# Optimization experiments

Hardware: AMD Instinct MI355X
Metric: run time of the kernel (lower is better)

## Reference

```python
import jax, jax.numpy as jnp
import numpy as np

C, B, F, O, DK = 10, 8192, 256, 64, 5


def setup_inputs() -> dict:
    key = jax.random.key(0)
    ks = jax.random.split(key, 7)
    x = jax.random.normal(ks[0], (B, F), jnp.float32)
    y = jax.random.normal(ks[1], (B, C), jnp.float32)
    # kaiming-uniform-like init scales
    w_key = jax.random.normal(ks[2], (C, 1, 1, DK), jnp.float32) * 0.5
    w_query = jax.random.normal(ks[3], (C, 1, DK), jnp.float32) * 0.5
    w_value = jax.random.normal(ks[4], (C, 1, 1), jnp.float32) * 0.5
    weight = jax.random.normal(ks[5], (C, 1, F, O), jnp.float32) * (1.0 / np.sqrt(F))
    bias = jax.random.normal(ks[6], (C, 1, O), jnp.float32) * 0.1
    return {"x": x, "y": y, "w_key": w_key, "w_query": w_query,
            "w_value": w_value, "weight": weight, "bias": bias}


def reference(x, y, w_key, w_query, w_value, weight, bias):
    # x: [B,F] (first=True -> conceptually [1,B,F]); y: [B,C]
    yt = y.T                                             # [C,B]
    querys = yt[..., None] * w_query                     # [C,B,1]*[C,1,DK] -> [C,B,DK]
    # keys[c,b,f,k] = x[b,f] * w_key[c,k]; attn_scores[c,b,f] = sum_k keys*querys
    #              = x[b,f] * (w_key[c] . querys[c,b])  (rank-1 structure, fused)
    kq = jnp.einsum('ck,cbk->cb', w_key.reshape(w_key.shape[0], -1), querys)  # [C,B]
    # mean over batch dim, then softmax over features
    scores_avg = jnp.einsum('bf,cb->cf', x, kq) / x.shape[0]  # [C,F]
    sm = jax.nn.softmax(scores_avg, axis=-1)                  # [C,F]
    attn = sm / jnp.max(sm, axis=-1, keepdims=True)           # [C,F] max-normalized
    values = x[None, :, :] * w_value                          # [1,B,F]*[C,1,1] -> [C,B,F]
    weighted = values * attn[:, None, :]                      # [C,B,F]
    # (weighted[...,None,:] @ weight).squeeze() + bias -> [C,B,O]
    out = jnp.einsum('cbf,cfo->cbo', weighted, weight[:, 0]) + bias  # bias [C,1,O]
    return out
```

## Files before the change

### kernel.cpp

```cpp
#include <hip/hip_runtime.h>
#include <hip/hip_bf16.h>

#define C_ 10
#define B_ 8192
#define F_ 256
#define O_ 64
#define DK_ 5
#define NBLK1 256
#define NG2   16

typedef __attribute__((ext_vector_type(8))) short short8;
typedef __attribute__((ext_vector_type(4))) float floatx4;

static __device__ __forceinline__ unsigned short f2bf(float f) {
    union { float f; unsigned u; } v; v.f = f;
    unsigned r = v.u + 0x7fffu + ((v.u >> 16) & 1u);
    return (unsigned short)(r >> 16);
}

__global__ __launch_bounds__(256) void k1_reduce(const float* __restrict__ x,
                                                 const float* __restrict__ y,
                                                 float* __restrict__ G_part) {
    __shared__ float xl[32 * F_];
    __shared__ float yl[32 * C_];
    const int b0 = blockIdx.x * 32;
    const int t  = threadIdx.x;

    for (int i = t; i < 32 * C_; i += 256) yl[i] = y[b0 * C_ + i];

    const int r  = t >> 6;
    const int f4 = (t & 63) * 4;
#pragma unroll
    for (int j = 0; j < 8; ++j) {
        int row = r + 4 * j;
        float4 v = *(const float4*)(x + (size_t)(b0 + row) * F_ + f4);
        *(float4*)(xl + row * F_ + f4) = v;
    }
    __syncthreads();

    float acc[C_];
#pragma unroll
    for (int c = 0; c < C_; ++c) acc[c] = 0.f;

#pragma unroll 8
    for (int b = 0; b < 32; ++b) {
        float xv = xl[b * F_ + t];
#pragma unroll
        for (int c = 0; c < C_; ++c) acc[c] = fmaf(yl[b * C_ + c], xv, acc[c]);
    }

    float* gp = G_part + (size_t)blockIdx.x * C_ * F_ + t;
#pragma unroll
    for (int c = 0; c < C_; ++c) gp[c * F_] = acc[c];
}

__global__ __launch_bounds__(256) void k1b_reduce(const float* __restrict__ G_part,
                                                  const float* __restrict__ weight,
                                                  float* __restrict__ G2,
                                                  unsigned short* __restrict__ WTB) {
    const int c = (int)blockIdx.x >> 4;
    const int g = (int)blockIdx.x & 15;
    const int t = threadIdx.x;

    const float* gp = G_part + (size_t)(g * 16) * C_ * F_ + c * F_ + t;
    float a0 = 0.f, a1 = 0.f, a2 = 0.f, a3 = 0.f;
#pragma unroll
    for (int i = 0; i < 16; i += 4) {
        a0 += gp[(size_t)(i + 0) * C_ * F_];
        a1 += gp[(size_t)(i + 1) * C_ * F_];
        a2 += gp[(size_t)(i + 2) * C_ * F_];
        a3 += gp[(size_t)(i + 3) * C_ * F_];
    }
    G2[(size_t)g * C_ * F_ + c * F_ + t] = (a0 + a1) + (a2 + a3);

    const int o  = t & 63;
    const int fq = t >> 6;
    const int f0 = g * 16 + fq * 4;
    const float* wsrc = weight + (size_t)c * F_ * O_;
    ushort4 v;
    v.x = f2bf(wsrc[(f0 + 0) * O_ + o]);
    v.y = f2bf(wsrc[(f0 + 1) * O_ + o]);
    v.z = f2bf(wsrc[(f0 + 2) * O_ + o]);
    v.w = f2bf(wsrc[(f0 + 3) * O_ + o]);
    char* wb = (char*)(WTB + (size_t)c * O_ * F_);
    *(ushort4*)(wb + o * 512 + ((2 * f0) ^ ((o & 7) << 4))) = v;
}

__global__ __launch_bounds__(256) void k3_fused(const float* __restrict__ x,
                                                const float* __restrict__ G2,
                                                const float* __restrict__ w_key,
                                                const float* __restrict__ w_query,
                                                const float* __restrict__ w_value,
                                                const float* __restrict__ bias,
                                                const unsigned short* __restrict__ WTB,
                                                float* __restrict__ out) {
    __shared__ unsigned short wt[O_ * F_];
    __shared__ float a2s[F_];
    __shared__ float wred[4];
    const int c  = blockIdx.y;
    const int b0 = blockIdx.x * 64;
    const int t  = threadIdx.x;
    const int w  = t >> 6;
    const int l  = t & 63;
    const int lr = l & 15;
    const int lg = l >> 4;

    const float* xr = x + (size_t)(b0 + w * 16 + lr) * F_;
    float4 araw0[8], araw1[8];
#pragma unroll
    for (int k0 = 0; k0 < 8; ++k0) {
        araw0[k0] = *(const float4*)(xr + k0 * 32 + lg * 8);
        araw1[k0] = *(const float4*)(xr + k0 * 32 + lg * 8 + 4);
    }
    const float bo_r = bias[c * O_ + lr];
    const float bo1  = bias[c * O_ + 16 + lr];
    const float bo2  = bias[c * O_ + 32 + lr];
    const float bo3  = bias[c * O_ + 48 + lr];

    {
        const short8* src = (const short8*)(WTB + (size_t)c * O_ * F_);
        short8* dst = (short8*)wt;
#pragma unroll
        for (int j = 0; j < 8; ++j) dst[t + 256 * j] = src[t + 256 * j];
    }

    {
        const float* gp = G2 + c * F_ + t;
        float g0 = 0.f, g1 = 0.f, g2 = 0.f, g3 = 0.f;
#pragma unroll
        for (int i = 0; i < NG2; i += 4) {
            g0 += gp[(size_t)(i + 0) * C_ * F_];
            g1 += gp[(size_t)(i + 1) * C_ * F_];
            g2 += gp[(size_t)(i + 2) * C_ * F_];
            g3 += gp[(size_t)(i + 3) * C_ * F_];
        }
        float g = (g0 + g1) + (g2 + g3);

        float s = 0.f;
#pragma unroll
        for (int k = 0; k < DK_; ++k) s += w_key[c * DK_ + k] * w_query[c * DK_ + k];

        float z = s * g * (1.0f / (float)B_);
        float m = z;
#pragma unroll
        for (int off = 32; off >= 1; off >>= 1) m = fmaxf(m, __shfl_xor(m, off));
        if ((t & 63) == 0) wred[t >> 6] = m;
        __syncthreads();
        float mm = fmaxf(fmaxf(wred[0], wred[1]), fmaxf(wred[2], wred[3]));
        a2s[t] = expf(z - mm) * w_value[c];
    }
    __syncthreads();

    short8 afr[8];
#pragma unroll
    for (int k0 = 0; k0 < 8; ++k0) {
        const int kk = k0 * 32 + lg * 8;
        float4 s0 = *(const float4*)(a2s + kk);
        float4 s1 = *(const float4*)(a2s + kk + 4);
        short8 fr;
        fr[0] = (short)f2bf(araw0[k0].x * s0.x);
        fr[1] = (short)f2bf(araw0[k0].y * s0.y);
        fr[2] = (short)f2bf(araw0[k0].z * s0.z);
        fr[3] = (short)f2bf(araw0[k0].w * s0.w);
        fr[4] = (short)f2bf(araw1[k0].x * s1.x);
        fr[5] = (short)f2bf(araw1[k0].y * s1.y);
        fr[6] = (short)f2bf(araw1[k0].z * s1.z);
        fr[7] = (short)f2bf(araw1[k0].w * s1.w);
        afr[k0] = fr;
    }

    floatx4 acc[4];
    acc[0] = (floatx4){bo_r, bo_r, bo_r, bo_r};
    acc[1] = (floatx4){bo1, bo1, bo1, bo1};
    acc[2] = (floatx4){bo2, bo2, bo2, bo2};
    acc[3] = (floatx4){bo3, bo3, bo3, bo3};

#pragma unroll
    for (int k0 = 0; k0 < 8; ++k0) {
#pragma unroll
        for (int n = 0; n < 4; ++n) {
            int o = n * 16 + lr;
            int byte = o * 512 + ((k0 * 64 + lg * 16) ^ ((o & 7) << 4));
            short8 bf = *(const short8*)((const char*)wt + byte);
            acc[n] = __builtin_amdgcn_mfma_f32_16x16x32_bf16(afr[k0], bf, acc[n], 0, 0, 0);
        }
    }

#pragma unroll
    for (int n = 0; n < 4; ++n) {
        int col = n * 16 + lr;
#pragma unroll
        for (int r = 0; r < 4; ++r) {
            int row = b0 + w * 16 + lg * 4 + r;
            out[((size_t)c * B_ + row) * O_ + col] = acc[n][r];
        }
    }
}

extern "C" void kernel_launch(void* const* d_in, const int* in_sizes, int n_in,
                              void* d_out, int out_size, void* d_ws, size_t ws_size,
                              hipStream_t stream) {
    const float* x       = (const float*)d_in[0];
    const float* y       = (const float*)d_in[1];
    const float* w_key   = (const float*)d_in[2];
    const float* w_query = (const float*)d_in[3];
    const float* w_value = (const float*)d_in[4];
    const float* weight  = (const float*)d_in[5];
    const float* bias    = (const float*)d_in[6];
    float* out = (float*)d_out;

    char* ws = (char*)d_ws;
    float*          G_part = (float*)ws;
    float*          G2     = G_part + (size_t)NBLK1 * C_ * F_;
    unsigned short* WTB    = (unsigned short*)(G2 + (size_t)NG2 * C_ * F_);

    k1_reduce<<<NBLK1, 256, 0, stream>>>(x, y, G_part);
    k1b_reduce<<<C_ * NG2, 256, 0, stream>>>(G_part, weight, G2, WTB);
    dim3 g3(B_ / 64, C_);
    k3_fused<<<g3, 256, 0, stream>>>(x, G2, w_key, w_query, w_value, bias, WTB, out);
}
```

Baseline: 29.16 us.

## Merge reduction and weight-conversion kernels, move partial-sum reduction into main kernel

Cuts the pipeline from three launches to two. The first kernel now handles the batch reduction with 64 blocks of 128 rows each (reading x directly instead of staging it in LDS), and its extra blocks do the weight-to-bf16 transpose. The intermediate second-stage reduction kernel is removed; each block of the main kernel sums the 64 partials itself using its four waves and a shared-memory combine. This saves a launch and its dependency gap, at the cost of fewer, longer reduction blocks and redundant partial-sum reads in every block of the main kernel.

```diff
diff --git a/kernel.cpp b/kernel.cpp
--- a/kernel.cpp
+++ b/kernel.cpp
@@ -6,8 +6,7 @@
 #define F_ 256
 #define O_ 64
 #define DK_ 5
-#define NBLK1 256
-#define NG2   16
+#define P_ 64
 
 typedef __attribute__((ext_vector_type(8))) short short8;
 typedef __attribute__((ext_vector_type(4))) float floatx4;
@@ -18,83 +17,64 @@
     return (unsigned short)(r >> 16);
 }
 
-__global__ __launch_bounds__(256) void k1_reduce(const float* __restrict__ x,
-                                                 const float* __restrict__ y,
-                                                 float* __restrict__ G_part) {
-    __shared__ float xl[32 * F_];
-    __shared__ float yl[32 * C_];
-    const int b0 = blockIdx.x * 32;
-    const int t  = threadIdx.x;
-
-    for (int i = t; i < 32 * C_; i += 256) yl[i] = y[b0 * C_ + i];
-
-    const int r  = t >> 6;
-    const int f4 = (t & 63) * 4;
-#pragma unroll
-    for (int j = 0; j < 8; ++j) {
-        int row = r + 4 * j;
-        float4 v = *(const float4*)(x + (size_t)(b0 + row) * F_ + f4);
-        *(float4*)(xl + row * F_ + f4) = v;
-    }
-    __syncthreads();
-
-    float acc[C_];
-#pragma unroll
-    for (int c = 0; c < C_; ++c) acc[c] = 0.f;
-
+__global__ __launch_bounds__(256) void kA(const float* __restrict__ x,
+                                          const float* __restrict__ y,
+                                          const float* __restrict__ weight,
+                                          float* __restrict__ G_part,
+                                          unsigned short* __restrict__ WTB) {
+    const int t = threadIdx.x;
+    if (blockIdx.x < P_) {
+        __shared__ float yl[128 * C_];
+        const int b0 = blockIdx.x * 128;
+        for (int i = t; i < 128 * C_; i += 256) yl[i] = y[b0 * C_ + i];
+        __syncthreads();
+
+        float acc[C_];
+#pragma unroll
+        for (int c = 0; c < C_; ++c) acc[c] = 0.f;
+
+        const float* xp = x + (size_t)b0 * F_ + t;
 #pragma unroll 8
-    for (int b = 0; b < 32; ++b) {
-        float xv = xl[b * F_ + t];
-#pragma unroll
-        for (int c = 0; c < C_; ++c) acc[c] = fmaf(yl[b * C_ + c], xv, acc[c]);
-    }
-
-    float* gp = G_part + (size_t)blockIdx.x * C_ * F_ + t;
-#pragma unroll
-    for (int c = 0; c < C_; ++c) gp[c * F_] = acc[c];
-}
-
-__global__ __launch_bounds__(256) void k1b_reduce(const float* __restrict__ G_part,
-                                                  const float* __restrict__ weight,
-                                                  float* __restrict__ G2,
-                                                  unsigned short* __restrict__ WTB) {
-    const int c = (int)blockIdx.x >> 4;
-    const int g = (int)blockIdx.x & 15;
-    const int t = threadIdx.x;
-
-    const float* gp = G_part + (size_t)(g * 16) * C_ * F_ + c * F_ + t;
-    float a0 = 0.f, a1 = 0.f, a2 = 0.f, a3 = 0.f;
-#pragma unroll
-    for (int i = 0; i < 16; i += 4) {
-        a0 += gp[(size_t)(i + 0) * C_ * F_];
-        a1 += gp[(size_t)(i + 1) * C_ * F_];
-        a2 += gp[(size_t)(i + 2) * C_ * F_];
-        a3 += gp[(size_t)(i + 3) * C_ * F_];
-    }
-    G2[(size_t)g * C_ * F_ + c * F_ + t] = (a0 + a1) + (a2 + a3);
-
-    const int o  = t & 63;
-    const int fq = t >> 6;
-    const int f0 = g * 16 + fq * 4;
-    const float* wsrc = weight + (size_t)c * F_ * O_;
-    ushort4 v;
-    v.x = f2bf(wsrc[(f0 + 0) * O_ + o]);
-    v.y = f2bf(wsrc[(f0 + 1) * O_ + o]);
-    v.z = f2bf(wsrc[(f0 + 2) * O_ + o]);
-    v.w = f2bf(wsrc[(f0 + 3) * O_ + o]);
-    char* wb = (char*)(WTB + (size_t)c * O_ * F_);
-    *(ushort4*)(wb + o * 512 + ((2 * f0) ^ ((o & 7) << 4))) = v;
-}
-
-__global__ __launch_bounds__(256) void k3_fused(const float* __restrict__ x,
-                                                const float* __restrict__ G2,
-                                                const float* __restrict__ w_key,
-                                                const float* __restrict__ w_query,
-                                                const float* __restrict__ w_value,
-                                                const float* __restrict__ bias,
-                                                const unsigned short* __restrict__ WTB,
-                                                float* __restrict__ out) {
+        for (int b = 0; b < 128; ++b) {
+            float xv = xp[(size_t)b * F_];
+#pragma unroll
+            for (int c = 0; c < C_; ++c) acc[c] = fmaf(yl[b * C_ + c], xv, acc[c]);
+        }
+
+        float* gp = G_part + (size_t)blockIdx.x * C_ * F_ + t;
+#pragma unroll
+        for (int c = 0; c < C_; ++c) gp[c * F_] = acc[c];
+    } else {
+        const int sp   = (int)blockIdx.x - P_;
+        const int cc   = sp >> 2;
+        const int part = sp & 3;
+        const int o  = t & 63;
+        const int fq = t >> 6;
+        const float* wsrc = weight + (size_t)cc * F_ * O_;
+        char* wb = (char*)(WTB + (size_t)cc * O_ * F_);
+#pragma unroll
+        for (int gi = 0; gi < 4; ++gi) {
+            int f0 = part * 64 + gi * 16 + fq * 4;
+            ushort4 v;
+            v.x = f2bf(wsrc[(f0 + 0) * O_ + o]);
+            v.y = f2bf(wsrc[(f0 + 1) * O_ + o]);
+            v.z = f2bf(wsrc[(f0 + 2) * O_ + o]);
+            v.w = f2bf(wsrc[(f0 + 3) * O_ + o]);
+            *(ushort4*)(wb + o * 512 + ((2 * f0) ^ ((o & 7) << 4))) = v;
+        }
+    }
+}
+
+__global__ __launch_bounds__(256) void kB(const float* __restrict__ x,
+                                          const float* __restrict__ G_part,
+                                          const float* __restrict__ w_key,
+                                          const float* __restrict__ w_query,
+                                          const float* __restrict__ w_value,
+                                          const float* __restrict__ bias,
+                                          const unsigned short* __restrict__ WTB,
+                                          float* __restrict__ out) {
     __shared__ unsigned short wt[O_ * F_];
+    __shared__ float red[4 * F_];
     __shared__ float a2s[F_];
     __shared__ float wred[4];
     const int c  = blockIdx.y;
@@ -112,10 +92,24 @@
         araw0[k0] = *(const float4*)(xr + k0 * 32 + lg * 8);
         araw1[k0] = *(const float4*)(xr + k0 * 32 + lg * 8 + 4);
     }
-    const float bo_r = bias[c * O_ + lr];
-    const float bo1  = bias[c * O_ + 16 + lr];
-    const float bo2  = bias[c * O_ + 32 + lr];
-    const float bo3  = bias[c * O_ + 48 + lr];
+    const float bo0 = bias[c * O_ + lr];
+    const float bo1 = bias[c * O_ + 16 + lr];
+    const float bo2 = bias[c * O_ + 32 + lr];
+    const float bo3 = bias[c * O_ + 48 + lr];
+
+    {
+        const float* gp = G_part + ((size_t)(w * 16) * C_ + c) * F_ + l;
+        float s0 = 0.f, s1 = 0.f, s2 = 0.f, s3 = 0.f;
+#pragma unroll
+        for (int p = 0; p < 16; ++p) {
+            const float* q = gp + (size_t)p * C_ * F_;
+            s0 += q[0]; s1 += q[64]; s2 += q[128]; s3 += q[192];
+        }
+        red[w * F_ + l]       = s0;
+        red[w * F_ + 64 + l]  = s1;
+        red[w * F_ + 128 + l] = s2;
+        red[w * F_ + 192 + l] = s3;
+    }
 
     {
         const short8* src = (const short8*)(WTB + (size_t)c * O_ * F_);
@@ -123,18 +117,10 @@
 #pragma unroll
         for (int j = 0; j < 8; ++j) dst[t + 256 * j] = src[t + 256 * j];
     }
+    __syncthreads();
 
     {
-        const float* gp = G2 + c * F_ + t;
-        float g0 = 0.f, g1 = 0.f, g2 = 0.f, g3 = 0.f;
-#pragma unroll
-        for (int i = 0; i < NG2; i += 4) {
-            g0 += gp[(size_t)(i + 0) * C_ * F_];
-            g1 += gp[(size_t)(i + 1) * C_ * F_];
-            g2 += gp[(size_t)(i + 2) * C_ * F_];
-            g3 += gp[(size_t)(i + 3) * C_ * F_];
-        }
-        float g = (g0 + g1) + (g2 + g3);
+        float g = (red[t] + red[F_ + t]) + (red[2 * F_ + t] + red[3 * F_ + t]);
 
         float s = 0.f;
 #pragma unroll
@@ -170,7 +156,7 @@
     }
 
     floatx4 acc[4];
-    acc[0] = (floatx4){bo_r, bo_r, bo_r, bo_r};
+    acc[0] = (floatx4){bo0, bo0, bo0, bo0};
     acc[1] = (floatx4){bo1, bo1, bo1, bo1};
     acc[2] = (floatx4){bo2, bo2, bo2, bo2};
     acc[3] = (floatx4){bo3, bo3, bo3, bo3};
@@ -190,9 +176,9 @@
     for (int n = 0; n < 4; ++n) {
         int col = n * 16 + lr;
 #pragma unroll
-        for (int r = 0; r < 4; ++r) {
-            int row = b0 + w * 16 + lg * 4 + r;
-            out[((size_t)c * B_ + row) * O_ + col] = acc[n][r];
+        for (int r2 = 0; r2 < 4; ++r2) {
+            int row = b0 + w * 16 + lg * 4 + r2;
+            out[((size_t)c * B_ + row) * O_ + col] = acc[n][r2];
         }
     }
 }
@@ -211,11 +197,9 @@
 
     char* ws = (char*)d_ws;
     float*          G_part = (float*)ws;
-    float*          G2     = G_part + (size_t)NBLK1 * C_ * F_;
-    unsigned short* WTB    = (unsigned short*)(G2 + (size_t)NG2 * C_ * F_);
-
-    k1_reduce<<<NBLK1, 256, 0, stream>>>(x, y, G_part);
-    k1b_reduce<<<C_ * NG2, 256, 0, stream>>>(G_part, weight, G2, WTB);
-    dim3 g3(B_ / 64, C_);
-    k3_fused<<<g3, 256, 0, stream>>>(x, G2, w_key, w_query, w_value, bias, WTB, out);
-}
+    unsigned short* WTB    = (unsigned short*)(G_part + (size_t)P_ * C_ * F_);
+
+    kA<<<P_ + C_ * 4, 256, 0, stream>>>(x, y, weight, G_part, WTB);
+    dim3 g(B_ / 64, C_);
+    kB<<<g, 256, 0, stream>>>(x, G_part, w_key, w_query, w_value, bias, WTB, out);
+}
```

After: 32.88 us. +12.7%, slower.
